# Optimization experiments

Measured on AMD Instinct MI355X. Metric: run time of the kernel, lower is better.

## Reference

```python
import jax, jax.numpy as jnp
import numpy as np
import math

# Fixed order-36 Hadamard matrix transcribed from the module's get_had36().
_H36 = [
    "++++++++++++++++++-+++++++++++++++++",
    "++++-+---++---+-+++-++-+---++---+-++",
    "+++++-+---++---+-+++-++-+---++---+-+",
    "++++++-+---++---+-+++-++-+---++---+-",
    "+-+++++-+---++---++-++-++-+---++---+",
    "++-+++++-+---++---++-++-++-+---++---",
    "+-+-+++++-+---++--+-+-++-++-+---++--",
    "+--+-+++++-+---++-+--+-++-++-+---++-",
    "+---+-+++++-+---+++---+-++-++-+---++",
    "++---+-+++++-+---+++---+-++-++-+---+",
    "+++---+-+++++-+---+++---+-++-++-+---",
    "+-++---+-+++++-+--+-++---+-++-++-+--",
    "+--++---+-+++++-+-+--++---+-++-++-+-",
    "+---++---+-+++++-++---++---+-++-++-+",
    "++---++---+-+++++-++---++---+-++-++-",
    "+-+---++---+-++++++-+---++---+-++-++",
    "++-+---++---+-++++++-+---++---+-++-+",
    "+++-+---++---+-++++++-+---++---+-++-",
    "-+++++++++++++++++------------------",
    "+-++-+---++---+-++----+-+++--+++-+--",
    "++-++-+---++---+-+-----+-+++--+++-+-",
    "+++-++-+---++---+-------+-+++--+++-+",
    "+-++-++-+---++---+-+-----+-+++--+++-",
    "++-++-++-+---++-----+-----+-+++--+++",
    "+-+-++-++-+---++---+-+-----+-+++--++",
    "+--+-++-++-+---++--++-+-----+-+++--+",
    "+---+-++-++-+---++-+++-+-----+-+++--",
    "++---+-++-++-+---+--+++-+-----+-+++-",
    "+++---+-++-++-+------+++-+-----+-+++",
    "+-++---+-++-++-+---+--+++-+-----+-++",
    "+--++---+-++-++-+--++--+++-+-----+-+",
    "+---++---+-++-++-+-+++--+++-+-----+-",
    "++---++---+-++-++---+++--+++-+-----+",
    "+-+---++---+-++-++-+-+++--+++-+-----",
    "++-+---++---+-++-+--+-+++--+++-+----",
    "+++-+---++---+-++----+-+++--+++-+---",
]

def _had36():
    m = np.array([[1.0 if c == '+' else -1.0 for c in row] for row in _H36],
                 dtype=np.float32)
    return jnp.asarray(m)

def _fwht_kron(x, had_k):
    """matmul_hadU: FWHT butterfly on the power-of-2 factor of n, then a
    dense matmul with the fixed order-K Hadamard block, scaled by 1/sqrt(n)."""
    orig_shape = x.shape
    n = orig_shape[-1]            # 2304 = 36 * 64
    K = had_k.shape[0]            # 36
    t = x.reshape(-1, n, 1)
    while t.shape[1] > K:         # log2(n // K) = 6 static butterfly stages
        mid, last = t.shape[1], t.shape[2]
        t = t.reshape(-1, mid // 2, 2, last)
        a, b = t[:, :, 0, :], t[:, :, 1, :]
        t = jnp.concatenate([a + b, a - b], axis=-1)  # (B, mid//2, 2*last)
    # t: (B, K, n//K); mix the size-36 factor with the fixed Hadamard matrix
    t = jnp.einsum('kj,bjm->bkm', had_k, t)
    return t.reshape(orig_shape) * (1.0 / math.sqrt(n))

def setup_inputs() -> dict:
    key = jax.random.key(0)
    x = jax.random.normal(key, (4, 8192, 2304), dtype=jnp.float32)
    return {"x": x, "had_k": _had36()}

def reference(x, had_k):
    return _fwht_kron(x, had_k)
```

## Files before the change

kernel.cpp:

```cpp
#include <hip/hip_runtime.h>
#include <stdint.h>


constexpr uint64_t neg_mask(const char* s) {
    uint64_t m = 0;
    for (int j = 0; j < 36; ++j)
        if (s[j] == '-') m |= (1ull << j);
    return m;
}

constexpr uint64_t NEG[36] = {
    neg_mask("++++++++++++++++++-+++++++++++++++++"),
    neg_mask("++++-+---++---+-+++-++-+---++---+-++"),
    neg_mask("+++++-+---++---+-+++-++-+---++---+-+"),
    neg_mask("++++++-+---++---+-+++-++-+---++---+-"),
    neg_mask("+-+++++-+---++---++-++-++-+---++---+"),
    neg_mask("++-+++++-+---++---++-++-++-+---++---"),
    neg_mask("+-+-+++++-+---++--+-+-++-++-+---++--"),
    neg_mask("+--+-+++++-+---++-+--+-++-++-+---++-"),
    neg_mask("+---+-+++++-+---+++---+-++-++-+---++"),
    neg_mask("++---+-+++++-+---+++---+-++-++-+---+"),
    neg_mask("+++---+-+++++-+---+++---+-++-++-+---"),
    neg_mask("+-++---+-+++++-+--+-++---+-++-++-+--"),
    neg_mask("+--++---+-+++++-+-+--++---+-++-++-+-"),
    neg_mask("+---++---+-+++++-++---++---+-++-++-+"),
    neg_mask("++---++---+-+++++-++---++---+-++-++-"),
    neg_mask("+-+---++---+-++++++-+---++---+-++-++"),
    neg_mask("++-+---++---+-++++++-+---++---+-++-+"),
    neg_mask("+++-+---++---+-++++++-+---++---+-++-"),
    neg_mask("-+++++++++++++++++------------------"),
    neg_mask("+-++-+---++---+-++----+-+++--+++-+--"),
    neg_mask("++-++-+---++---+-+-----+-+++--+++-+-"),
    neg_mask("+++-++-+---++---+-------+-+++--+++-+"),
    neg_mask("+-++-++-+---++---+-+-----+-+++--+++-"),
    neg_mask("++-++-++-+---++-----+-----+-+++--+++"),
    neg_mask("+-+-++-++-+---++---+-+-----+-+++--++"),
    neg_mask("+--+-++-++-+---++--++-+-----+-+++--+"),
    neg_mask("+---+-++-++-+---++-+++-+-----+-+++--"),
    neg_mask("++---+-++-++-+---+--+++-+-----+-+++-"),
    neg_mask("+++---+-++-++-+------+++-+-----+-+++"),
    neg_mask("+-++---+-++-++-+---+--+++-+-----+-++"),
    neg_mask("+--++---+-++-++-+--++--+++-+-----+-+"),
    neg_mask("+---++---+-++-++-+-+++--+++-+-----+-"),
    neg_mask("++---++---+-++-++---+++--+++-+-----+"),
    neg_mask("+-+---++---+-++-++-+-+++--+++-+-----"),
    neg_mask("++-+---++---+-++-+--+-+++--+++-+----"),
    neg_mask("+++-+---++---+-++----+-+++--+++-+---"),
};

#define ROWLEN 2304

__global__ __launch_bounds__(256) void had_kernel(const float* __restrict__ x,
                                                  float* __restrict__ out,
                                                  int n_rows) {
    const int tid  = threadIdx.x;
    const int wave = tid >> 6;
    const int lane = tid & 63;
    const int q    = lane & 31;
    const int rsub = lane >> 5;

    const long long row = (long long)blockIdx.x * 8 + wave * 2 + rsub;
    if (row >= n_rows) return;

    const float* xr = x + row * ROWLEN + 2 * q;

    float v0[36], v1[36];
#pragma unroll
    for (int j = 0; j < 36; ++j) {
        float2 t = *(const float2*)(xr + j * 64);
        v0[j] = t.x;
        v1[j] = t.y;
    }

#pragma unroll
    for (int j = 0; j < 36; ++j) {
        float a = v0[j], b = v1[j];
        v0[j] = a + b;
        v1[j] = a - b;
    }

#pragma unroll
    for (int p = 0; p < 5; ++p) {
        const int mask = 1 << p;
        const float s = (q & mask) ? -1.0f : 1.0f;
#pragma unroll
        for (int j = 0; j < 36; ++j) {
            float p0 = __shfl_xor(v0[j], mask, 64);
            float p1 = __shfl_xor(v1[j], mask, 64);
            v0[j] = fmaf(v0[j], s, p0);
            v1[j] = fmaf(v1[j], s, p1);
        }
    }

    float S0 = 0.0f, S1 = 0.0f;
#pragma unroll
    for (int j = 0; j < 36; ++j) {
        S0 += v0[j];
        S1 += v1[j];
    }
    const float inv48 = 1.0f / 48.0f;
    const float m2_48 = -2.0f / 48.0f;
    S0 *= inv48;
    S1 *= inv48;

    float* yr = out + row * ROWLEN + 2 * q;

#pragma unroll
    for (int k = 0; k < 36; ++k) {
        const uint64_t m = NEG[k];
        float n0 = 0.0f, n1 = 0.0f;
#pragma unroll
        for (int j = 0; j < 36; ++j) {
            if ((m >> j) & 1) {
                n0 += v0[j];
                n1 += v1[j];
            }
        }
        float y0 = fmaf(n0, m2_48, S0);
        float y1 = fmaf(n1, m2_48, S1);
        *(float2*)(yr + k * 64) = make_float2(y0, y1);
    }
}

extern "C" void kernel_launch(void* const* d_in, const int* in_sizes, int n_in,
                              void* d_out, int out_size, void* d_ws, size_t ws_size,
                              hipStream_t stream) {
    const float* x = (const float*)d_in[0];
    float* out = (float*)d_out;
    const int n_rows = in_sizes[0] / ROWLEN;
    const int rows_per_block = 8;
    const int grid = (n_rows + rows_per_block - 1) / rows_per_block;
    hipLaunchKernelGGL(had_kernel, dim3(grid), dim3(256), 0, stream, x, out, n_rows);
}
```

Baseline: 484.7 us.

## Assign one row per wave with scalar loads and permlane32 swap stage

Each wave now processes one full row with one float per lane per segment instead of two half-rows with float2 loads. Register use is roughly halved and launch bounds now request higher occupancy. The sixth butterfly stage uses a cross-half lane swap, via permlane32_swap when the builtin exists and a shuffle otherwise, and the row sum uses four independent accumulators. The 36x36 mix sums whichever sign set is smaller per row, which cuts adds. The cost is an extra cross-lane stage and narrower 4-byte global accesses in place of 8-byte vector ones.

```diff
diff --git a/kernel.cpp b/kernel.cpp
--- a/kernel.cpp
+++ b/kernel.cpp
@@ -50,75 +50,83 @@
 
 #define ROWLEN 2304
 
-__global__ __launch_bounds__(256) void had_kernel(const float* __restrict__ x,
-                                                  float* __restrict__ out,
-                                                  int n_rows) {
+__global__ __launch_bounds__(256, 8) void had_kernel(const float* __restrict__ x,
+                                                     float* __restrict__ out,
+                                                     int n_rows) {
     const int tid  = threadIdx.x;
     const int wave = tid >> 6;
     const int lane = tid & 63;
-    const int q    = lane & 31;
-    const int rsub = lane >> 5;
 
-    const long long row = (long long)blockIdx.x * 8 + wave * 2 + rsub;
+    const long long row = (long long)blockIdx.x * 4 + wave;
     if (row >= n_rows) return;
 
-    const float* xr = x + row * ROWLEN + 2 * q;
+    const float* xr = x + row * (long long)ROWLEN + lane;
 
-    float v0[36], v1[36];
+    float v[36];
 #pragma unroll
-    for (int j = 0; j < 36; ++j) {
-        float2 t = *(const float2*)(xr + j * 64);
-        v0[j] = t.x;
-        v1[j] = t.y;
-    }
-
-#pragma unroll
-    for (int j = 0; j < 36; ++j) {
-        float a = v0[j], b = v1[j];
-        v0[j] = a + b;
-        v1[j] = a - b;
-    }
+    for (int j = 0; j < 36; ++j) v[j] = xr[j * 64];
 
 #pragma unroll
     for (int p = 0; p < 5; ++p) {
         const int mask = 1 << p;
-        const float s = (q & mask) ? -1.0f : 1.0f;
+        const float s = (lane & mask) ? -1.0f : 1.0f;
 #pragma unroll
         for (int j = 0; j < 36; ++j) {
-            float p0 = __shfl_xor(v0[j], mask, 64);
-            float p1 = __shfl_xor(v1[j], mask, 64);
-            v0[j] = fmaf(v0[j], s, p0);
-            v1[j] = fmaf(v1[j], s, p1);
+            float pv = __shfl_xor(v[j], mask, 64);
+            v[j] = fmaf(v[j], s, pv);
         }
     }
 
-    float S0 = 0.0f, S1 = 0.0f;
+    {
+        const float s = (lane & 32) ? -1.0f : 1.0f;
+#if __has_builtin(__builtin_amdgcn_permlane32_swap)
+        const bool hi = (lane & 32) != 0;
+        typedef unsigned int uint2v __attribute__((ext_vector_type(2)));
 #pragma unroll
-    for (int j = 0; j < 36; ++j) {
-        S0 += v0[j];
-        S1 += v1[j];
+        for (int j = 0; j < 36; ++j) {
+            unsigned int b = __float_as_uint(v[j]);
+            uint2v r = __builtin_amdgcn_permlane32_swap(b, b, false, false);
+            float pv = __uint_as_float(hi ? r.x : r.y);
+            v[j] = fmaf(v[j], s, pv);
+        }
+#else
+#pragma unroll
+        for (int j = 0; j < 36; ++j) {
+            float pv = __shfl_xor(v[j], 32, 64);
+            v[j] = fmaf(v[j], s, pv);
+        }
+#endif
     }
-    const float inv48 = 1.0f / 48.0f;
-    const float m2_48 = -2.0f / 48.0f;
-    S0 *= inv48;
-    S1 *= inv48;
 
-    float* yr = out + row * ROWLEN + 2 * q;
+    float s0 = 0.0f, s1 = 0.0f, s2 = 0.0f, s3 = 0.0f;
+#pragma unroll
+    for (int j = 0; j < 36; j += 4) {
+        s0 += v[j];
+        s1 += v[j + 1];
+        s2 += v[j + 2];
+        s3 += v[j + 3];
+    }
+    const float S = (s0 + s1) + (s2 + s3);
+
+    const float S48   = S * (1.0f / 48.0f);
+    const float mS48  = -S48;
+    const float c_neg = -2.0f / 48.0f;
+    const float c_pos =  2.0f / 48.0f;
+
+    float* yr = out + row * (long long)ROWLEN + lane;
 
 #pragma unroll
     for (int k = 0; k < 36; ++k) {
-        const uint64_t m = NEG[k];
-        float n0 = 0.0f, n1 = 0.0f;
+        const uint64_t m  = NEG[k];
+        const int      pc = __builtin_popcountll(m);
+        const uint64_t msel = (pc <= 18) ? m : (~m & ((1ull << 36) - 1));
+        float acc = 0.0f;
 #pragma unroll
         for (int j = 0; j < 36; ++j) {
-            if ((m >> j) & 1) {
-                n0 += v0[j];
-                n1 += v1[j];
-            }
+            if ((msel >> j) & 1) acc += v[j];
         }
-        float y0 = fmaf(n0, m2_48, S0);
-        float y1 = fmaf(n1, m2_48, S1);
-        *(float2*)(yr + k * 64) = make_float2(y0, y1);
+        const float y = (pc <= 18) ? fmaf(acc, c_neg, S48) : fmaf(acc, c_pos, mS48);
+        yr[k * 64] = y;
     }
 }
 
@@ -128,7 +136,7 @@
     const float* x = (const float*)d_in[0];
     float* out = (float*)d_out;
     const int n_rows = in_sizes[0] / ROWLEN;
-    const int rows_per_block = 8;
+    const int rows_per_block = 4;
     const int grid = (n_rows + rows_per_block - 1) / rows_per_block;
     hipLaunchKernelGGL(had_kernel, dim3(grid), dim3(256), 0, stream, x, out, n_rows);
 }
```

New measurement: 483.6 us. No clear change (-0.2%).
